# Kernel optimization log

Hardware: AMD Instinct MI355X
Metric: run time of the kernel (lower is better)

The kernel has to match this reference:

```python
import jax, jax.numpy as jnp
import numpy as np

EMB_DIM = 512
QKV_DIM = 512
NUM_HEADS = 8
HEAD_DIM = QKV_DIM // NUM_HEADS
NUM_LANDMARKS = 64
N_ITER = 6


def setup_inputs() -> dict:
    key = jax.random.key(0)
    ks = jax.random.split(key, 9)
    s = 1.0 / np.sqrt(EMB_DIM)
    return {
        "x": jax.random.normal(ks[0], (4, 8192, EMB_DIM), dtype=jnp.float32),
        "Wq": jax.random.normal(ks[1], (EMB_DIM, QKV_DIM), dtype=jnp.float32) * s,
        "bq": jnp.zeros((QKV_DIM,), dtype=jnp.float32),
        "Wk": jax.random.normal(ks[2], (EMB_DIM, QKV_DIM), dtype=jnp.float32) * s,
        "bk": jnp.zeros((QKV_DIM,), dtype=jnp.float32),
        "Wv": jax.random.normal(ks[3], (EMB_DIM, QKV_DIM), dtype=jnp.float32) * s,
        "bv": jnp.zeros((QKV_DIM,), dtype=jnp.float32),
        "Wo": jax.random.normal(ks[4], (QKV_DIM, EMB_DIM), dtype=jnp.float32) * s,
        "bo": jnp.zeros((EMB_DIM,), dtype=jnp.float32),
    }


def _split_heads(x):
    bs, sl, _ = x.shape
    return x.reshape(bs, sl, NUM_HEADS, HEAD_DIM).transpose(0, 2, 1, 3)


def _iterative_inv(K):
    # K: [bs, h, L, L]; Newton-Schulz pseudo-inverse, 'original' init
    L = K.shape[-1]
    I = jnp.eye(L, dtype=K.dtype)
    V = K.swapaxes(-1, -2) / jnp.max(jnp.sum(K, axis=-2))
    for _ in range(N_ITER):
        KV = jnp.matmul(K, V)
        V = jnp.matmul(0.25 * V, 13.0 * I - jnp.matmul(KV, 15.0 * I - jnp.matmul(KV, 7.0 * I - KV)))
    return V


def reference(x, Wq, bq, Wk, bk, Wv, bv, Wo, bo):
    bs, seqlen, _ = x.shape
    # seqlen chosen divisible by NUM_LANDMARKS, so no padding branch
    full_len = seqlen
    q = _split_heads(x @ Wq + bq)
    k = _split_heads(x @ Wk + bk)
    v = _split_heads(x @ Wv + bv)
    scale = 1.0 / np.sqrt(np.sqrt(HEAD_DIM))
    q = q * scale
    k = k * scale

    seg = full_len // NUM_LANDMARKS
    q_land = q.reshape(bs, NUM_HEADS, NUM_LANDMARKS, seg, HEAD_DIM).mean(axis=-2)
    k_land = k.reshape(bs, NUM_HEADS, NUM_LANDMARKS, seg, HEAD_DIM).mean(axis=-2)

    kernel_1 = jax.nn.softmax(jnp.einsum('bhsd,bhld->bhsl', q, k_land), axis=-1)  # [bs,h,S,L]
    kernel_2 = jax.nn.softmax(jnp.einsum('bhld,bhmd->bhlm', q_land, k_land), axis=-1)  # [bs,h,L,L]
    kernel_3 = jax.nn.softmax(jnp.einsum('bhld,bhsd->bhls', q_land, k), axis=-1)  # [bs,h,L,S]

    out = jnp.matmul(jnp.matmul(kernel_1, _iterative_inv(kernel_2)), jnp.matmul(kernel_3, v))  # [bs,h,S,d]
    out = out.transpose(0, 2, 1, 3).reshape(bs, seqlen, QKV_DIM)
    return out @ Wo + bo
```

## Files before the change

kernel.cpp:

```cpp
#include <hip/hip_runtime.h>

#define BS 4
#define SEQL 8192
#define EMB 512
#define NH 8
#define HD 64
#define LM 64
#define SEG 128
#define BH (BS*NH)
#define NCH 16
#define CHS (SEQL/NCH)
#define QSCALE 0.35355339059327373f

typedef unsigned short u16;
typedef __bf16 bf16_t;
typedef __attribute__((ext_vector_type(8))) __bf16 bf16x8;
typedef __attribute__((ext_vector_type(4))) float f32x4;

#define MFMA16(a, b, c) __builtin_amdgcn_mfma_f32_16x16x32_bf16((a), (b), (c), 0, 0, 0)

__device__ __forceinline__ float bf2f(u16 u) {
  return __uint_as_float(((unsigned int)u) << 16);
}
__device__ __forceinline__ u16 f2bf(float f) {
  unsigned int u = __float_as_uint(f);
  u += 0x7fffu + ((u >> 16) & 1u);
  return (u16)(u >> 16);
}
__device__ __forceinline__ float load1_any(const void* p, size_t idx, int isf32) {
  return isf32 ? ((const float*)p)[idx] : bf2f(((const u16*)p)[idx]);
}
__device__ __forceinline__ void load4_any(const void* p, size_t idx, int isf32, float* dst) {
  if (isf32) {
    float4 v = *reinterpret_cast<const float4*>((const float*)p + idx);
    dst[0] = v.x; dst[1] = v.y; dst[2] = v.z; dst[3] = v.w;
  } else {
    ushort4 v = *reinterpret_cast<const ushort4*>((const u16*)p + idx);
    dst[0] = bf2f(v.x); dst[1] = bf2f(v.y); dst[2] = bf2f(v.z); dst[3] = bf2f(v.w);
  }
}
__device__ __forceinline__ void ld8_bf(const void* p, size_t idx, int isf32, u16* o) {
  if (isf32) {
    const float* f = (const float*)p + idx;
    float4 a = *reinterpret_cast<const float4*>(f);
    float4 b = *reinterpret_cast<const float4*>(f + 4);
    o[0] = f2bf(a.x); o[1] = f2bf(a.y); o[2] = f2bf(a.z); o[3] = f2bf(a.w);
    o[4] = f2bf(b.x); o[5] = f2bf(b.y); o[6] = f2bf(b.z); o[7] = f2bf(b.w);
  } else {
    *reinterpret_cast<int4*>(o) = *reinterpret_cast<const int4*>((const u16*)p + idx);
  }
}

__device__ __forceinline__ void async16(const void* g, void* l) {
  __builtin_amdgcn_global_load_lds(
      (const __attribute__((address_space(1))) void*)g,
      (__attribute__((address_space(3))) void*)l, 16, 0, 0);
}

__global__ __launch_bounds__(256) void probe_kernel(const void* x, int* flag) {
  __shared__ int cnt;
  if (threadIdx.x == 0) cnt = 0;
  __syncthreads();
  const u16* p = (const u16*)x;
  int c = 0;
  for (int j = 0; j < 16; j++) {
    u16 u = p[(size_t)(threadIdx.x * 16 + j) * 2];
    int e = (u >> 7) & 0xFF;
    if (e >= 134) c++;
  }
  atomicAdd(&cnt, c);
  __syncthreads();
  if (threadIdx.x == 0) flag[0] = (cnt > 256) ? 1 : 0;
}

__global__ __launch_bounds__(256) void prep_wt_kernel(
    const void* Wq, const void* Wk, const void* Wv, const void* Wo, const int* flag,
    u16* __restrict__ WqT, u16* __restrict__ WkT, u16* __restrict__ WvT, u16* __restrict__ WoT)
{
  __shared__ u16 Ws[64 * 72];
  const int id = blockIdx.x;
  const int z = id >> 6, tile = id & 63;
  const int k0 = (tile >> 3) * 64, n0 = (tile & 7) * 64;
  const void* W = (z == 0) ? Wq : (z == 1) ? Wk : (z == 2) ? Wv : Wo;
  u16* WT = (z == 0) ? WqT : (z == 1) ? WkT : (z == 2) ? WvT : WoT;
  const int isf32 = flag[0];
  const int t = threadIdx.x;
  const int r = t >> 2, cq = (t & 3) * 16;
  u16 tmp[8];
  #pragma unroll
  for (int u = 0; u < 2; u++) {
    ld8_bf(W, (size_t)(k0 + r) * EMB + n0 + cq + 8 * u, isf32, tmp);
    *reinterpret_cast<int4*>(&Ws[r * 72 + cq + 8 * u]) = *reinterpret_cast<int4*>(tmp);
  }
  __syncthreads();
  const int nn = t >> 2, kq = (t & 3) * 16;
  #pragma unroll
  for (int u = 0; u < 2; u++) {
    u16 o[8];
    #pragma unroll
    for (int j = 0; j < 8; j++) o[j] = Ws[(kq + 8 * u + j) * 72 + nn];
    *reinterpret_cast<int4*>(&WT[(size_t)(n0 + nn) * EMB + k0 + kq + 8 * u]) =
        *reinterpret_cast<int4*>(o);
  }
}

__global__ __launch_bounds__(256) void xpart_kernel(const void* x, const int* flag,
                                                    float* __restrict__ xpart,
                                                    u16* __restrict__ xb16) {
  __shared__ float red[512];
  const int blk = blockIdx.x;
  const int bl = blk >> 3, ch = blk & 7;
  const int t = threadIdx.x;
  const int isf32 = flag[0];
  const int rg = t >> 7;
  const int c4 = (t & 127) * 4;
  const size_t base = ((size_t)bl * SEG + ch * 16) * EMB;
  float s0 = 0.f, s1 = 0.f, s2 = 0.f, s3 = 0.f;
  for (int r = rg; r < 16; r += 2) {
    size_t idx = base + (size_t)r * EMB + c4;
    if (isf32) {
      float4 v = *reinterpret_cast<const float4*>((const float*)x + idx);
      ushort4 ob;
      ob.x = f2bf(v.x); ob.y = f2bf(v.y); ob.z = f2bf(v.z); ob.w = f2bf(v.w);
      *reinterpret_cast<ushort4*>(&xb16[idx]) = ob;
      s0 += v.x; s1 += v.y; s2 += v.z; s3 += v.w;
    } else {
      ushort4 v = *reinterpret_cast<const ushort4*>((const u16*)x + idx);
      s0 += bf2f(v.x); s1 += bf2f(v.y); s2 += bf2f(v.z); s3 += bf2f(v.w);
    }
  }
  if (rg == 0) {
    red[c4] = s0; red[c4 + 1] = s1; red[c4 + 2] = s2; red[c4 + 3] = s3;
  }
  __syncthreads();
  if (rg == 1) {
    red[c4] += s0; red[c4 + 1] += s1; red[c4 + 2] += s2; red[c4 + 3] += s3;
  }
  __syncthreads();
  if (t < 128) {
    float4 o;
    o.x = red[t * 4]; o.y = red[t * 4 + 1]; o.z = red[t * 4 + 2]; o.w = red[t * 4 + 3];
    *reinterpret_cast<float4*>(&xpart[(size_t)blk * 512 + t * 4]) = o;
  }
}

__global__ __launch_bounds__(256) void xmean_reduce_kernel(
    const float* __restrict__ xpart, float* __restrict__ xmean) {
  const int bl = blockIdx.x;
  const int t = threadIdx.x;
  const int c = t * 2;
  float s0 = 0.f, s1 = 0.f;
  #pragma unroll
  for (int ch = 0; ch < 8; ch++) {
    const float* p = &xpart[((size_t)(bl * 8 + ch)) * 512 + c];
    s0 += p[0]; s1 += p[1];
  }
  xmean[(size_t)bl * EMB + c]     = s0 * (1.0f / SEG);
  xmean[(size_t)bl * EMB + c + 1] = s1 * (1.0f / SEG);
}

__global__ __launch_bounds__(256) void lm_proj_kernel(
    const float* __restrict__ xmean,
    const void* Wq, const void* bq, const void* Wk, const void* bk,
    const int* flag, float* __restrict__ qL, float* __restrict__ kL,
    u16* __restrict__ qLb, u16* __restrict__ kLb)
{
  __shared__ float As[64 * 17];
  __shared__ float Bs[16 * 64];
  const int t = threadIdx.x;
  const int m0 = blockIdx.x * 64, n0 = blockIdx.y * 64, z = blockIdx.z;
  const void* W    = z ? Wk : Wq;
  const void* bias = z ? bk : bq;
  float* dst       = z ? kL : qL;
  u16*   dstb      = z ? kLb : qLb;
  const int isf32 = flag[0];
  const int tx = t & 15, ty = t >> 4;
  const int arow = t >> 2, akk = (t & 3) << 2;
  const int brow = t >> 4, bcol = (t & 15) << 2;
  float acc[4][4] = {};
  for (int k0 = 0; k0 < EMB; k0 += 16) {
    float4 av = *reinterpret_cast<const float4*>(xmean + (size_t)(m0 + arow) * EMB + k0 + akk);
    As[arow * 17 + akk + 0] = av.x;
    As[arow * 17 + akk + 1] = av.y;
    As[arow * 17 + akk + 2] = av.z;
    As[arow * 17 + akk + 3] = av.w;
    load4_any(W, (size_t)(k0 + brow) * EMB + n0 + bcol, isf32, &Bs[brow * 64 + bcol]);
    __syncthreads();
    #pragma unroll
    for (int kk = 0; kk < 16; kk++) {
      float a[4], b[4];
      #pragma unroll
      for (int i = 0; i < 4; i++) a[i] = As[(ty * 4 + i) * 17 + kk];
      #pragma unroll
      for (int j = 0; j < 4; j++) b[j] = Bs[kk * 64 + tx * 4 + j];
      #pragma unroll
      for (int i = 0; i < 4; i++)
        #pragma unroll
        for (int j = 0; j < 4; j++)
          acc[i][j] = fmaf(a[i], b[j], acc[i][j]);
    }
    __syncthreads();
  }
  #pragma unroll
  for (int i = 0; i < 4; i++) {
    int m = m0 + ty * 4 + i;
    int b = m >> 6, l = m & 63;
    #pragma unroll
    for (int j = 0; j < 4; j++) {
      int n = n0 + tx * 4 + j;
      int h = n >> 6, d = n & 63;
      float c = (acc[i][j] + load1_any(bias, n, isf32)) * QSCALE;
      size_t idx = (size_t)((b * NH + h) * LM + l) * HD + d;
      dst[idx] = c;
      dstb[idx] = f2bf(c);
    }
  }
}

__global__ __launch_bounds__(256, 2) void proj_qkv_fused_kernel(
    const void* x, const u16* __restrict__ xb16, const u16* __restrict__ WqT,
    const u16* __restrict__ WkT, const u16* __restrict__ WvT,
    const void* bq, const void* bk, const void* bv, const int* flag,
    u16* __restrict__ Qb, u16* __restrict__ Kb, u16* __restrict__ VbT)
{
  __shared__ u16 smem[2 * 128 * 64 + 2 * 3 * 64 * 64];
  u16* As = smem;
  u16* Bs = smem + 2 * 128 * 64;
  const int t = threadIdx.x;
  const int orig = blockIdx.x;
  const int swz  = (orig & 7) * 256 + (orig >> 3);
  const int h    = swz & 7;
  const int m0   = (swz >> 3) * 128;
  const int n0   = h * 64;
  const int isf32 = flag[0];
  const u16* xs = isf32 ? xb16 : (const u16*)x;
  const int w = t >> 6, lane = t & 63, q = lane >> 4, c = lane & 15;
  const int wm = (w >> 1) * 64, wn = (w & 1) * 32;
  const int row8 = lane >> 3;
  const int csw  = ((lane & 7) ^ row8) * 8;

  f32x4 acc[3][4][2];
  f32x4 z4 = {0.f, 0.f, 0.f, 0.f};
  #pragma unroll
  for (int z = 0; z < 3; z++)
    #pragma unroll
    for (int mi = 0; mi < 4; mi++) { acc[z][mi][0] = z4; acc[z][mi][1] = z4; }

  #pragma unroll
  for (int u = 0; u < 4; u++) {
    int ca = u * 4 + w;
    async16(&xs[(size_t)(m0 + ca * 8 + row8) * EMB + 0 + csw], &As[ca * 512]);
  }
  #pragma unroll
  for (int u = 0; u < 6; u++) {
    int cb = u * 4 + w, z = cb >> 3, r8 = cb & 7;
    const u16* Wt = (z == 0) ? WqT : (z == 1) ? WkT : WvT;
    async16(&Wt[(size_t)(n0 + r8 * 8 + row8) * EMB + 0 + csw],
            &Bs[z * 4096 + r8 * 512]);
  }
  __syncthreads();

  for (int tt = 0; tt < 8; tt++) {
    const int cur = tt & 1;
    if (tt < 7) {
      const int k1 = (tt + 1) * 64;
      const int nb = (cur ^ 1);
      #pragma unroll
      for (int u = 0; u < 4; u++) {
        int ca = u * 4 + w;
        async16(&xs[(size_t)(m0 + ca * 8 + row8) * EMB + k1 + csw],
                &As[nb * 8192 + ca * 512]);
      }
      #pragma unroll
      for (int u = 0; u < 6; u++) {
        int cb = u * 4 + w, z = cb >> 3, r8 = cb & 7;
        const u16* Wt = (z == 0) ? WqT : (z == 1) ? WkT : WvT;
        async16(&Wt[(size_t)(n0 + r8 * 8 + row8) * EMB + k1 + csw],
                &Bs[nb * 12288 + z * 4096 + r8 * 512]);
      }
    }
    #pragma unroll
    for (int kk = 0; kk < 64; kk += 32) {
      const int u0 = ((((kk >> 3) + q) ^ (c & 7))) * 8;
      bf16x8 af[4];
      #pragma unroll
      for (int mi = 0; mi < 4; mi++)
        af[mi] = *reinterpret_cast<const bf16x8*>(
            &As[cur * 8192 + (wm + mi * 16 + c) * 64 + u0]);
      #pragma unroll
      for (int z = 0; z < 3; z++) {
        bf16x8 b0v = *reinterpret_cast<const bf16x8*>(
            &Bs[cur * 12288 + z * 4096 + (wn + c) * 64 + u0]);
        bf16x8 b1v = *reinterpret_cast<const bf16x8*>(
            &Bs[cur * 12288 + z * 4096 + (wn + 16 + c) * 64 + u0]);
        #pragma unroll
        for (int mi = 0; mi < 4; mi++) {
          acc[z][mi][0] = MFMA16(af[mi], b0v, acc[z][mi][0]);
          acc[z][mi][1] = MFMA16(af[mi], b1v, acc[z][mi][1]);
        }
      }
    }
    __syncthreads();
  }

  float bb[3][2];
  #pragma unroll
  for (int z = 0; z < 3; z++) {
    const void* bias = (z == 0) ? bq : (z == 1) ? bk : bv;
    bb[z][0] = load1_any(bias, n0 + wn + c, isf32);
    bb[z][1] = load1_any(bias, n0 + wn + 16 + c, isf32);
  }
  const int b = m0 >> 13, s0t = m0 & (SEQL - 1);

  #pragma unroll
  for (int z = 0; z < 2; z++) {
    u16* dst = z ? Kb : Qb;
    #pragma unroll
    for (int mi = 0; mi < 4; mi++)
      #pragma unroll
      for (int i = 0; i < 4; i++) {
        int s = s0t + wm + mi * 16 + q * 4 + i;
        size_t rowb = ((size_t)((b * NH + h) * SEQL + s)) * HD;
        dst[rowb + wn + c]      = f2bf((acc[z][mi][0][i] + bb[z][0]) * QSCALE);
        dst[rowb + wn + 16 + c] = f2bf((acc[z][mi][1][i] + bb[z][1]) * QSCALE);
      }
  }

  __syncthreads();
  #pragma unroll
  for (int mi = 0; mi < 4; mi++)
    #pragma unroll
    for (int i = 0; i < 4; i++) {
      int ml = wm + mi * 16 + q * 4 + i;
      smem[(wn + c) * 136 + ml]      = f2bf(acc[2][mi][0][i] + bb[2][0]);
      smem[(wn + 16 + c) * 136 + ml] = f2bf(acc[2][mi][1][i] + bb[2][1]);
    }
  __syncthreads();
  const int nl = t >> 2, cq2 = (t & 3) * 32;
  #pragma unroll
  for (int u = 0; u < 4; u++)
    *reinterpret_cast<int4*>(&VbT[((size_t)((b * NH + h) * HD + nl)) * SEQL + s0t + cq2 + 8 * u]) =
        *reinterpret_cast<int4*>(&smem[nl * 136 + cq2 + 8 * u]);
}

__global__ __launch_bounds__(256) void k2_softmax_kernel(
    const float* __restrict__ qL, const float* __restrict__ kL,
    float* __restrict__ K2, float* __restrict__ cs)
{
  __shared__ float qs[64 * 65], ks[64 * 65], ps[64 * 65];
  const int t = threadIdx.x, bh = blockIdx.x;
  const int r = t >> 2, cb = (t & 3) << 4;
  #pragma unroll
  for (int i = 0; i < 16; i++) {
    qs[r * 65 + cb + i] = qL[((size_t)bh * LM + r) * HD + cb + i];
    ks[r * 65 + cb + i] = kL[((size_t)bh * LM + r) * HD + cb + i];
  }
  __syncthreads();
  float lg[16] = {};
  for (int d = 0; d < HD; d++) {
    float a = qs[r * 65 + d];
    #pragma unroll
    for (int i = 0; i < 16; i++) lg[i] = fmaf(a, ks[(cb + i) * 65 + d], lg[i]);
  }
  float m = lg[0];
  #pragma unroll
  for (int i = 1; i < 16; i++) m = fmaxf(m, lg[i]);
  m = fmaxf(m, __shfl_xor(m, 1));
  m = fmaxf(m, __shfl_xor(m, 2));
  float s = 0.f;
  #pragma unroll
  for (int i = 0; i < 16; i++) { lg[i] = __expf(lg[i] - m); s += lg[i]; }
  s += __shfl_xor(s, 1);
  s += __shfl_xor(s, 2);
  const float inv = 1.0f / s;
  #pragma unroll
  for (int i = 0; i < 16; i++) {
    float p = lg[i] * inv;
    ps[r * 65 + cb + i] = p;
    K2[((size_t)bh * LM + r) * LM + cb + i] = p;
  }
  __syncthreads();
  if (t < 64) {
    float c = 0.f;
    for (int rr = 0; rr < 64; rr++) c += ps[rr * 65 + t];
    cs[bh * LM + t] = c;
  }
}

__device__ __forceinline__ void mm_split(const u16* Ah, const u16* Al,
                                         const u16* Bh, const u16* Bl,
                                         int w, int lane, f32x4* out)
{
  const int q = lane >> 4, c = lane & 15;
  bf16x8 ah[2], al[2];
  #pragma unroll
  for (int k2 = 0; k2 < 2; k2++) {
    ah[k2] = *reinterpret_cast<const bf16x8*>(&Ah[(w * 16 + c) * 72 + k2 * 32 + q * 8]);
    al[k2] = *reinterpret_cast<const bf16x8*>(&Al[(w * 16 + c) * 72 + k2 * 32 + q * 8]);
  }
  #pragma unroll
  for (int nb = 0; nb < 4; nb++) {
    f32x4 acc = {0.f, 0.f, 0.f, 0.f};
    #pragma unroll
    for (int k2 = 0; k2 < 2; k2++) {
      bf16x8 bh_ = *reinterpret_cast<const bf16x8*>(&Bh[(nb * 16 + c) * 72 + k2 * 32 + q * 8]);
      bf16x8 bl_ = *reinterpret_cast<const bf16x8*>(&Bl[(nb * 16 + c) * 72 + k2 * 32 + q * 8]);
      acc = MFMA16(ah[k2], bh_, acc);
      acc = MFMA16(ah[k2], bl_, acc);
      acc = MFMA16(al[k2], bh_, acc);
    }
    out[nb] = acc;
  }
}

__global__ __launch_bounds__(256) void ns_inverse_kernel(
    const float* __restrict__ K2, const float* __restrict__ cs,
    float* __restrict__ Vi)
{
  __shared__ u16 K2h[64 * 72], K2l[64 * 72];
  __shared__ u16 VAh[64 * 72], VAl[64 * 72];
  __shared__ u16 VTh[64 * 72], VTl[64 * 72];
  __shared__ u16 KVh[64 * 72], KVl[64 * 72];
  __shared__ u16 Th [64 * 72], Tl [64 * 72];
  __shared__ float red[256];
  const int t = threadIdx.x, bh = blockIdx.x;
  const int w = t >> 6, lane = t & 63, q = lane >> 4, c = lane & 15;

  float m = -1e30f;
  for (int i = t; i < BH * LM; i += 256) m = fmaxf(m, cs[i]);
  red[t] = m;
  __syncthreads();
  for (int off = 128; off; off >>= 1) {
    if (t < off) red[t] = fmaxf(red[t], red[t + off]);
    __syncthreads();
  }
  const float ginv = 1.0f / red[0];
  __syncthreads();

  {
    const int r = t >> 2, cb = (t & 3) << 4;
    #pragma unroll
    for (int i = 0; i < 16; i++) {
      float v = K2[((size_t)bh * LM + r) * LM + cb + i];
      u16 h1 = f2bf(v);
      K2h[r * 72 + cb + i] = h1;
      K2l[r * 72 + cb + i] = f2bf(v - bf2f(h1));
      float sv = v * ginv;
      u16 h2 = f2bf(sv);
      u16 l2 = f2bf(sv - bf2f(h2));
      VTh[r * 72 + cb + i] = h2;
      VTl[r * 72 + cb + i] = l2;
      VAh[(cb + i) * 72 + r] = h2;
      VAl[(cb + i) * 72 + r] = l2;
    }
  }
  __syncthreads();

  f32x4 o[4];
  for (int it = 0; it < 6; it++) {
    mm_split(K2h, K2l, VTh, VTl, w, lane, o);
    __syncthreads();
    #pragma unroll
    for (int nb = 0; nb < 4; nb++)
      #pragma unroll
      for (int i = 0; i < 4; i++) {
        const int row = w * 16 + q * 4 + i, col = nb * 16 + c;
        const float v = o[nb][i];
        const u16 h1 = f2bf(v);
        KVh[row * 72 + col] = h1;
        KVl[row * 72 + col] = f2bf(v - bf2f(h1));
        const float tv = (row == col ? 7.0f : 0.0f) - v;
        const u16 h2 = f2bf(tv);
        Th[col * 72 + row] = h2;
        Tl[col * 72 + row] = f2bf(tv - bf2f(h2));
      }
    __syncthreads();
    mm_split(KVh, KVl, Th, Tl, w, lane, o);
    __syncthreads();
    #pragma unroll
    for (int nb = 0; nb < 4; nb++)
      #pragma unroll
      for (int i = 0; i < 4; i++) {
        const int row = w * 16 + q * 4 + i, col = nb * 16 + c;
        const float tv = (row == col ? 15.0f : 0.0f) - o[nb][i];
        const u16 h2 = f2bf(tv);
        Th[col * 72 + row] = h2;
        Tl[col * 72 + row] = f2bf(tv - bf2f(h2));
      }
    __syncthreads();
    mm_split(KVh, KVl, Th, Tl, w, lane, o);
    __syncthreads();
    #pragma unroll
    for (int nb = 0; nb < 4; nb++)
      #pragma unroll
      for (int i = 0; i < 4; i++) {
        const int row = w * 16 + q * 4 + i, col = nb * 16 + c;
        const float tv = (row == col ? 13.0f : 0.0f) - o[nb][i];
        const u16 h2 = f2bf(tv);
        Th[col * 72 + row] = h2;
        Tl[col * 72 + row] = f2bf(tv - bf2f(h2));
      }
    __syncthreads();
    mm_split(VAh, VAl, Th, Tl, w, lane, o);
    __syncthreads();
    #pragma unroll
    for (int nb = 0; nb < 4; nb++)
      #pragma unroll
      for (int i = 0; i < 4; i++) {
        const int row = w * 16 + q * 4 + i, col = nb * 16 + c;
        const float v = 0.25f * o[nb][i];
        const u16 h1 = f2bf(v);
        const u16 l1 = f2bf(v - bf2f(h1));
        VAh[row * 72 + col] = h1;
        VAl[row * 72 + col] = l1;
        VTh[col * 72 + row] = h1;
        VTl[col * 72 + row] = l1;
        if (it == 5) Vi[((size_t)bh * LM + row) * LM + col] = v;
      }
    __syncthreads();
  }
}

__global__ __launch_bounds__(256) void k3v_kernel(
    const u16* __restrict__ qLb, const u16* __restrict__ Kb, const u16* __restrict__ VbT,
    float* __restrict__ pnum, float* __restrict__ pden)
{
  __shared__ u16 Ks[64 * 72], Vs[2][64 * 72], Ps[64 * 72];
  __shared__ float denL[256];
  const int t = threadIdx.x, ch = blockIdx.x, bh = blockIdx.y;
  const int w = t >> 6, lane = t & 63, q = lane >> 4, c = lane & 15;
  const int sr = t >> 2, sp = (t & 3) * 16;

  bf16x8 aq[4][2];
  #pragma unroll
  for (int mi = 0; mi < 4; mi++)
    #pragma unroll
    for (int k2 = 0; k2 < 2; k2++)
      aq[mi][k2] = *reinterpret_cast<const bf16x8*>(
          &qLb[((size_t)bh * LM + mi * 16 + c) * HD + k2 * 32 + q * 8]);

  f32x4 z4 = {0.f, 0.f, 0.f, 0.f};
  f32x4 nacc[4];
  #pragma unroll
  for (int mi = 0; mi < 4; mi++) nacc[mi] = z4;
  float denr[16] = {};

  int4 kr0, kr1, vr0, vr1;
  {
    const int s0 = ch * CHS;
    const u16* kp = &Kb[((size_t)bh * SEQL + s0 + sr) * HD + sp];
    const u16* vp = &VbT[((size_t)(bh * HD + sr)) * SEQL + s0 + sp];
    kr0 = *reinterpret_cast<const int4*>(kp);
    kr1 = *reinterpret_cast<const int4*>(kp + 8);
    vr0 = *reinterpret_cast<const int4*>(vp);
    vr1 = *reinterpret_cast<const int4*>(vp + 8);
  }

  for (int sub = 0; sub < 8; sub++) {
    const int cur = sub & 1;
    *reinterpret_cast<int4*>(&Ks[sr * 72 + sp])     = kr0;
    *reinterpret_cast<int4*>(&Ks[sr * 72 + sp + 8]) = kr1;
    *reinterpret_cast<int4*>(&Vs[cur][sr * 72 + sp])     = vr0;
    *reinterpret_cast<int4*>(&Vs[cur][sr * 72 + sp + 8]) = vr1;
    __syncthreads();
    f32x4 sacc[4];
    #pragma unroll
    for (int mi = 0; mi < 4; mi++) sacc[mi] = z4;
    bf16x8 bk0 = *reinterpret_cast<const bf16x8*>(&Ks[(w * 16 + c) * 72 + q * 8]);
    bf16x8 bk1 = *reinterpret_cast<const bf16x8*>(&Ks[(w * 16 + c) * 72 + 32 + q * 8]);
    #pragma unroll
    for (int mi = 0; mi < 4; mi++) {
      sacc[mi] = MFMA16(aq[mi][0], bk0, sacc[mi]);
      sacc[mi] = MFMA16(aq[mi][1], bk1, sacc[mi]);
    }
    #pragma unroll
    for (int mi = 0; mi < 4; mi++)
      #pragma unroll
      for (int i = 0; i < 4; i++) {
        float p = __expf(sacc[mi][i]);
        denr[mi * 4 + i] += p;
        Ps[(mi * 16 + q * 4 + i) * 72 + w * 16 + c] = f2bf(p);
      }
    __syncthreads();
    if (sub < 7) {
      const int s1 = ch * CHS + (sub + 1) * 64;
      const u16* kp = &Kb[((size_t)bh * SEQL + s1 + sr) * HD + sp];
      const u16* vp = &VbT[((size_t)(bh * HD + sr)) * SEQL + s1 + sp];
      kr0 = *reinterpret_cast<const int4*>(kp);
      kr1 = *reinterpret_cast<const int4*>(kp + 8);
      vr0 = *reinterpret_cast<const int4*>(vp);
      vr1 = *reinterpret_cast<const int4*>(vp + 8);
    }
    #pragma unroll
    for (int k2 = 0; k2 < 2; k2++) {
      bf16x8 bv_ = *reinterpret_cast<const bf16x8*>(&Vs[cur][(w * 16 + c) * 72 + k2 * 32 + q * 8]);
      #pragma unroll
      for (int mi = 0; mi < 4; mi++) {
        bf16x8 ap = *reinterpret_cast<const bf16x8*>(&Ps[(mi * 16 + c) * 72 + k2 * 32 + q * 8]);
        nacc[mi] = MFMA16(ap, bv_, nacc[mi]);
      }
    }
  }
  #pragma unroll
  for (int mi = 0; mi < 4; mi++)
    #pragma unroll
    for (int i = 0; i < 4; i++)
      pnum[(((size_t)bh * NCH + ch) * LM + mi * 16 + q * 4 + i) * HD + w * 16 + c] = nacc[mi][i];
  #pragma unroll
  for (int v = 0; v < 16; v++) {
    denr[v] += __shfl_xor(denr[v], 1);
    denr[v] += __shfl_xor(denr[v], 2);
    denr[v] += __shfl_xor(denr[v], 4);
    denr[v] += __shfl_xor(denr[v], 8);
  }
  if (c == 0) {
    #pragma unroll
    for (int mi = 0; mi < 4; mi++)
      #pragma unroll
      for (int i = 0; i < 4; i++)
        denL[w * 64 + mi * 16 + q * 4 + i] = denr[mi * 4 + i];
  }
  __syncthreads();
  if (t < 64)
    pden[((size_t)bh * NCH + ch) * LM + t] = denL[t] + denL[64 + t] + denL[128 + t] + denL[192 + t];
}

__global__ __launch_bounds__(256) void k3v_w2_kernel(
    const float* __restrict__ pnum, const float* __restrict__ pden,
    const float* __restrict__ Vi, u16* __restrict__ W2T)
{
  __shared__ float Vs[64 * 65], Ms[64 * 65], den[64];
  const int t = threadIdx.x, bh = blockIdx.x;
  const int r = t >> 2, cb = (t & 3) << 4;
  #pragma unroll
  for (int i = 0; i < 16; i++) Vs[r * 65 + cb + i] = Vi[((size_t)bh * LM + r) * LM + cb + i];
  float acc[16] = {};
  for (int ch = 0; ch < NCH; ch++) {
    const float* p = pnum + (((size_t)bh * NCH + ch) * LM + r) * HD + cb;
    #pragma unroll
    for (int i = 0; i < 16; i++) acc[i] += p[i];
  }
  if ((t & 3) == 0) {
    float d = 0.f;
    for (int ch = 0; ch < NCH; ch++) d += pden[((size_t)bh * NCH + ch) * LM + r];
    den[r] = d;
  }
  __syncthreads();
  const float dinv = 1.0f / den[r];
  #pragma unroll
  for (int i = 0; i < 16; i++) Ms[r * 65 + cb + i] = acc[i] * dinv;
  __syncthreads();
  float o[16] = {};
  for (int k = 0; k < 64; k++) {
    float a = Vs[r * 65 + k];
    #pragma unroll
    for (int i = 0; i < 16; i++) o[i] = fmaf(a, Ms[k * 65 + cb + i], o[i]);
  }
  #pragma unroll
  for (int i = 0; i < 16; i++)
    W2T[((size_t)bh * HD + cb + i) * LM + r] = f2bf(o[i]);
}

__global__ __launch_bounds__(256) void final_kernel(
    const u16* __restrict__ Qb, const u16* __restrict__ kLb, const u16* __restrict__ W2T,
    u16* __restrict__ pre)
{
  __shared__ u16 Ps[64 * 72];
  __shared__ float smL[256];
  const int t = threadIdx.x, st = blockIdx.x, bh = blockIdx.y;
  const int w = t >> 6, lane = t & 63, q = lane >> 4, c = lane & 15;
  const int sb = st * 64;

  bf16x8 aq[4][2], bkL[2], bw2[2];
  #pragma unroll
  for (int mi = 0; mi < 4; mi++)
    #pragma unroll
    for (int k2 = 0; k2 < 2; k2++)
      aq[mi][k2] = *reinterpret_cast<const bf16x8*>(
          &Qb[((size_t)bh * SEQL + sb + mi * 16 + c) * HD + k2 * 32 + q * 8]);
  #pragma unroll
  for (int k2 = 0; k2 < 2; k2++) {
    bkL[k2] = *reinterpret_cast<const bf16x8*>(
        &kLb[((size_t)bh * LM + w * 16 + c) * HD + k2 * 32 + q * 8]);
    bw2[k2] = *reinterpret_cast<const bf16x8*>(
        &W2T[((size_t)bh * HD + w * 16 + c) * LM + k2 * 32 + q * 8]);
  }

  f32x4 z4 = {0.f, 0.f, 0.f, 0.f};
  f32x4 sacc[4];
  #pragma unroll
  for (int mi = 0; mi < 4; mi++) sacc[mi] = z4;
  #pragma unroll
  for (int k2 = 0; k2 < 2; k2++)
    #pragma unroll
    for (int mi = 0; mi < 4; mi++)
      sacc[mi] = MFMA16(aq[mi][k2], bkL[k2], sacc[mi]);

  float p[16], dn[16];
  #pragma unroll
  for (int v = 0; v < 16; v++) {
    p[v] = __expf(sacc[v >> 2][v & 3]);
    dn[v] = p[v];
  }
  #pragma unroll
  for (int v = 0; v < 16; v++) {
    dn[v] += __shfl_xor(dn[v], 1);
    dn[v] += __shfl_xor(dn[v], 2);
    dn[v] += __shfl_xor(dn[v], 4);
    dn[v] += __shfl_xor(dn[v], 8);
  }
  if (c == 0) {
    #pragma unroll
    for (int mi = 0; mi < 4; mi++)
      #pragma unroll
      for (int i = 0; i < 4; i++)
        smL[w * 64 + mi * 16 + q * 4 + i] = dn[mi * 4 + i];
  }
  #pragma unroll
  for (int mi = 0; mi < 4; mi++)
    #pragma unroll
    for (int i = 0; i < 4; i++)
      Ps[(mi * 16 + q * 4 + i) * 72 + w * 16 + c] = f2bf(p[mi * 4 + i]);
  __syncthreads();

  f32x4 oacc[4];
  #pragma unroll
  for (int mi = 0; mi < 4; mi++) oacc[mi] = z4;
  #pragma unroll
  for (int k2 = 0; k2 < 2; k2++)
    #pragma unroll
    for (int mi = 0; mi < 4; mi++) {
      bf16x8 ap = *reinterpret_cast<const bf16x8*>(&Ps[(mi * 16 + c) * 72 + k2 * 32 + q * 8]);
      oacc[mi] = MFMA16(ap, bw2[k2], oacc[mi]);
    }
  #pragma unroll
  for (int mi = 0; mi < 4; mi++)
    #pragma unroll
    for (int i = 0; i < 4; i++) {
      int row = mi * 16 + q * 4 + i;
      float den = smL[row] + smL[64 + row] + smL[128 + row] + smL[192 + row];
      float v = oacc[mi][i] / den;
      pre[((size_t)((bh >> 3) * SEQL + sb + row)) * EMB + (bh & 7) * HD + w * 16 + c] = f2bf(v);
    }
}

__global__ __launch_bounds__(256, 2) void out_proj_kernel(
    const u16* __restrict__ pre, const u16* __restrict__ WoT, const void* bo,
    const int* flag, void* out)
{
  __shared__ u16 As[2 * 128 * 64];
  __shared__ u16 Bs[2 * 128 * 64];
  const int t = threadIdx.x;
  const int orig = blockIdx.x;
  const int swz  = (orig & 7) * 128 + (orig >> 3);
  const int m0 = (swz >> 2) * 128, n0 = (swz & 3) * 128;
  const int isf32 = flag[0];
  const int w = t >> 6, lane = t & 63, q = lane >> 4, c = lane & 15;
  const int wm = (w >> 1) * 64, wn = (w & 1) * 64;
  const int row8 = lane >> 3;
  const int colsw = ((lane & 7) ^ row8) * 8;

  f32x4 acc[4][4];
  f32x4 z4 = {0.f, 0.f, 0.f, 0.f};
  #pragma unroll
  for (int mi = 0; mi < 4; mi++)
    #pragma unroll
    for (int ni = 0; ni < 4; ni++) acc[mi][ni] = z4;

  #pragma unroll
  for (int u = 0; u < 4; u++) {
    int chA = u * 4 + w;
    async16(&pre[(size_t)(m0 + chA * 8 + row8) * EMB + 0 + colsw], &As[chA * 512]);
    async16(&WoT[(size_t)(n0 + chA * 8 + row8) * EMB + 0 + colsw], &Bs[chA * 512]);
  }
  __syncthreads();

  for (int tt = 0; tt < 8; tt++) {
    const int cur = tt & 1;
    if (tt < 7) {
      const int k1 = (tt + 1) * 64;
      #pragma unroll
      for (int u = 0; u < 4; u++) {
        int chA = u * 4 + w;
        async16(&pre[(size_t)(m0 + chA * 8 + row8) * EMB + k1 + colsw],
                &As[(cur ^ 1) * 8192 + chA * 512]);
        async16(&WoT[(size_t)(n0 + chA * 8 + row8) * EMB + k1 + colsw],
                &Bs[(cur ^ 1) * 8192 + chA * 512]);
      }
    }
    #pragma unroll
    for (int kk = 0; kk < 64; kk += 32) {
      const int u0 = ((((kk >> 3) + q) ^ (c & 7))) * 8;
      bf16x8 af[4], bfv[4];
      #pragma unroll
      for (int mi = 0; mi < 4; mi++)
        af[mi] = *reinterpret_cast<const bf16x8*>(&As[cur * 8192 + (wm + mi * 16 + c) * 64 + u0]);
      #pragma unroll
      for (int ni = 0; ni < 4; ni++)
        bfv[ni] = *reinterpret_cast<const bf16x8*>(&Bs[cur * 8192 + (wn + ni * 16 + c) * 64 + u0]);
      #pragma unroll
      for (int mi = 0; mi < 4; mi++)
        #pragma unroll
        for (int ni = 0; ni < 4; ni++)
          acc[mi][ni] = MFMA16(af[mi], bfv[ni], acc[mi][ni]);
    }
    __syncthreads();
  }
  float bb[4];
  #pragma unroll
  for (int ni = 0; ni < 4; ni++) bb[ni] = load1_any(bo, n0 + wn + ni * 16 + c, isf32);
  #pragma unroll
  for (int mi = 0; mi < 4; mi++)
    #pragma unroll
    for (int i = 0; i < 4; i++) {
      int m = m0 + wm + mi * 16 + q * 4 + i;
      #pragma unroll
      for (int ni = 0; ni < 4; ni++) {
        int n = n0 + wn + ni * 16 + c;
        float v = acc[mi][ni][i] + bb[ni];
        if (isf32) ((float*)out)[(size_t)m * EMB + n] = v;
        else       ((u16*)out)[(size_t)m * EMB + n] = f2bf(v);
      }
    }
}

extern "C" void kernel_launch(void* const* d_in, const int* in_sizes, int n_in,
                              void* d_out, int out_size, void* d_ws, size_t ws_size,
                              hipStream_t stream)
{
  (void)in_sizes; (void)n_in; (void)out_size; (void)ws_size;
  const void* x  = d_in[0];
  const void* Wq = d_in[1];
  const void* bq = d_in[2];
  const void* Wk = d_in[3];
  const void* bk = d_in[4];
  const void* Wv = d_in[5];
  const void* bv = d_in[6];
  const void* Wo = d_in[7];
  const void* bo = d_in[8];

  float* ws = (float*)d_ws;
  int*   flag  = (int*)ws;
  float* xmean = ws + 64;
  float* qL    = xmean + 131072;
  float* kL    = qL + 131072;
  float* K2    = kL + 131072;
  float* cs    = K2 + 131072;
  float* Vi    = cs + 2048;
  float* pnum  = Vi + 131072;
  float* pden  = pnum + 2097152;
  u16* WqT = (u16*)(pden + 32768);
  u16* WkT = WqT + 262144;
  u16* WvT = WkT + 262144;
  u16* WoT = WvT + 262144;
  u16* qLb = WoT + 262144;
  u16* kLb = qLb + 131072;
  u16* W2T = kLb + 131072;
  u16* Qb  = W2T + 131072;
  u16* Kb  = Qb + 16777216;
  u16* VbT = Kb + 16777216;
  u16* xb16 = VbT + 16777216;
  u16* pre = Kb;
  float* xpart = pnum;

  probe_kernel<<<1, 256, 0, stream>>>(x, flag);
  prep_wt_kernel<<<256, 256, 0, stream>>>(Wq, Wk, Wv, Wo, flag, WqT, WkT, WvT, WoT);
  xpart_kernel<<<2048, 256, 0, stream>>>(x, flag, xpart, xb16);
  xmean_reduce_kernel<<<256, 256, 0, stream>>>(xpart, xmean);
  lm_proj_kernel<<<dim3(4, 8, 2), 256, 0, stream>>>(xmean, Wq, bq, Wk, bk, flag, qL, kL, qLb, kLb);
  proj_qkv_fused_kernel<<<dim3(2048), 256, 0, stream>>>(
      x, xb16, WqT, WkT, WvT, bq, bk, bv, flag, Qb, Kb, VbT);
  k2_softmax_kernel<<<BH, 256, 0, stream>>>(qL, kL, K2, cs);
  ns_inverse_kernel<<<BH, 256, 0, stream>>>(K2, cs, Vi);
  k3v_kernel<<<dim3(NCH, BH), 256, 0, stream>>>(qLb, Kb, VbT, pnum, pden);
  k3v_w2_kernel<<<BH, 256, 0, stream>>>(pnum, pden, Vi, W2T);
  final_kernel<<<dim3(SEQL / 64, BH), 256, 0, stream>>>(Qb, kLb, W2T, pre);
  out_proj_kernel<<<dim3(1024), 256, 0, stream>>>(pre, WoT, bo, flag, d_out);
}
```

Before: 383.7 us.

## Stage epilogue stores through LDS for coalesced writes and double-buffer K in k3v

The k3v kernel gets a second K shared-memory buffer and two register prefetch sets, so loads for tile sub+2 are issued two tiles ahead. The final and out_proj kernels now write their results to padded shared memory first and then copy them to global memory with 16-byte vector stores, replacing scattered 2- or 4-byte per-lane writes. This is meant to cut write traffic inefficiency and hide global load latency, at the cost of more LDS, extra barriers and more registers, which could lower occupancy.

```diff
diff --git a/kernel.cpp b/kernel.cpp
--- a/kernel.cpp
+++ b/kernel.cpp
@@ -521,11 +521,22 @@
   }
 }
 
+struct KV2 { int4 k0, k1, v0, v1; };
+__device__ __forceinline__ void k3v_load(const u16* Kb, const u16* VbT, int bh,
+                                         int s0, int sr, int sp, KV2& r) {
+  const u16* kp = &Kb[((size_t)bh * SEQL + s0 + sr) * HD + sp];
+  const u16* vp = &VbT[((size_t)(bh * HD + sr)) * SEQL + s0 + sp];
+  r.k0 = *reinterpret_cast<const int4*>(kp);
+  r.k1 = *reinterpret_cast<const int4*>(kp + 8);
+  r.v0 = *reinterpret_cast<const int4*>(vp);
+  r.v1 = *reinterpret_cast<const int4*>(vp + 8);
+}
+
 __global__ __launch_bounds__(256) void k3v_kernel(
     const u16* __restrict__ qLb, const u16* __restrict__ Kb, const u16* __restrict__ VbT,
     float* __restrict__ pnum, float* __restrict__ pden)
 {
-  __shared__ u16 Ks[64 * 72], Vs[2][64 * 72], Ps[64 * 72];
+  __shared__ u16 Ks[2][64 * 72], Vs[2][64 * 72], Ps[64 * 72];
   __shared__ float denL[256];
   const int t = threadIdx.x, ch = blockIdx.x, bh = blockIdx.y;
   const int w = t >> 6, lane = t & 63, q = lane >> 4, c = lane & 15;
@@ -545,62 +556,55 @@
   for (int mi = 0; mi < 4; mi++) nacc[mi] = z4;
   float denr[16] = {};
 
-  int4 kr0, kr1, vr0, vr1;
-  {
-    const int s0 = ch * CHS;
-    const u16* kp = &Kb[((size_t)bh * SEQL + s0 + sr) * HD + sp];
-    const u16* vp = &VbT[((size_t)(bh * HD + sr)) * SEQL + s0 + sp];
-    kr0 = *reinterpret_cast<const int4*>(kp);
-    kr1 = *reinterpret_cast<const int4*>(kp + 8);
-    vr0 = *reinterpret_cast<const int4*>(vp);
-    vr1 = *reinterpret_cast<const int4*>(vp + 8);
-  }
-
-  for (int sub = 0; sub < 8; sub++) {
-    const int cur = sub & 1;
-    *reinterpret_cast<int4*>(&Ks[sr * 72 + sp])     = kr0;
-    *reinterpret_cast<int4*>(&Ks[sr * 72 + sp + 8]) = kr1;
-    *reinterpret_cast<int4*>(&Vs[cur][sr * 72 + sp])     = vr0;
-    *reinterpret_cast<int4*>(&Vs[cur][sr * 72 + sp + 8]) = vr1;
-    __syncthreads();
-    f32x4 sacc[4];
-    #pragma unroll
-    for (int mi = 0; mi < 4; mi++) sacc[mi] = z4;
-    bf16x8 bk0 = *reinterpret_cast<const bf16x8*>(&Ks[(w * 16 + c) * 72 + q * 8]);
-    bf16x8 bk1 = *reinterpret_cast<const bf16x8*>(&Ks[(w * 16 + c) * 72 + 32 + q * 8]);
-    #pragma unroll
-    for (int mi = 0; mi < 4; mi++) {
-      sacc[mi] = MFMA16(aq[mi][0], bk0, sacc[mi]);
-      sacc[mi] = MFMA16(aq[mi][1], bk1, sacc[mi]);
-    }
-    #pragma unroll
-    for (int mi = 0; mi < 4; mi++)
-      #pragma unroll
-      for (int i = 0; i < 4; i++) {
-        float p = __expf(sacc[mi][i]);
-        denr[mi * 4 + i] += p;
-        Ps[(mi * 16 + q * 4 + i) * 72 + w * 16 + c] = f2bf(p);
-      }
-    __syncthreads();
-    if (sub < 7) {
-      const int s1 = ch * CHS + (sub + 1) * 64;
-      const u16* kp = &Kb[((size_t)bh * SEQL + s1 + sr) * HD + sp];
-      const u16* vp = &VbT[((size_t)(bh * HD + sr)) * SEQL + s1 + sp];
-      kr0 = *reinterpret_cast<const int4*>(kp);
-      kr1 = *reinterpret_cast<const int4*>(kp + 8);
-      vr0 = *reinterpret_cast<const int4*>(vp);
-      vr1 = *reinterpret_cast<const int4*>(vp + 8);
-    }
-    #pragma unroll
-    for (int k2 = 0; k2 < 2; k2++) {
-      bf16x8 bv_ = *reinterpret_cast<const bf16x8*>(&Vs[cur][(w * 16 + c) * 72 + k2 * 32 + q * 8]);
-      #pragma unroll
-      for (int mi = 0; mi < 4; mi++) {
-        bf16x8 ap = *reinterpret_cast<const bf16x8*>(&Ps[(mi * 16 + c) * 72 + k2 * 32 + q * 8]);
-        nacc[mi] = MFMA16(ap, bv_, nacc[mi]);
-      }
-    }
-  }
+  KV2 rA, rB;
+  k3v_load(Kb, VbT, bh, ch * CHS + 0 * 64, sr, sp, rA);
+  k3v_load(Kb, VbT, bh, ch * CHS + 1 * 64, sr, sp, rB);
+
+#define K3V_SUB(SLOT, REGS, NEXTSUB)                                              \
+  {                                                                               \
+    *reinterpret_cast<int4*>(&Ks[SLOT][sr * 72 + sp])     = REGS.k0;              \
+    *reinterpret_cast<int4*>(&Ks[SLOT][sr * 72 + sp + 8]) = REGS.k1;              \
+    *reinterpret_cast<int4*>(&Vs[SLOT][sr * 72 + sp])     = REGS.v0;              \
+    *reinterpret_cast<int4*>(&Vs[SLOT][sr * 72 + sp + 8]) = REGS.v1;              \
+    __syncthreads();                                                              \
+    f32x4 sacc[4];                                                                \
+    _Pragma("unroll")                                                             \
+    for (int mi = 0; mi < 4; mi++) sacc[mi] = z4;                                 \
+    bf16x8 bk0 = *reinterpret_cast<const bf16x8*>(&Ks[SLOT][(w * 16 + c) * 72 + q * 8]);      \
+    bf16x8 bk1 = *reinterpret_cast<const bf16x8*>(&Ks[SLOT][(w * 16 + c) * 72 + 32 + q * 8]); \
+    _Pragma("unroll")                                                             \
+    for (int mi = 0; mi < 4; mi++) {                                              \
+      sacc[mi] = MFMA16(aq[mi][0], bk0, sacc[mi]);                                \
+      sacc[mi] = MFMA16(aq[mi][1], bk1, sacc[mi]);                                \
+    }                                                                             \
+    _Pragma("unroll")                                                             \
+    for (int mi = 0; mi < 4; mi++)                                                \
+      _Pragma("unroll")                                                           \
+      for (int i = 0; i < 4; i++) {                                               \
+        float p = __expf(sacc[mi][i]);                                            \
+        denr[mi * 4 + i] += p;                                                    \
+        Ps[(mi * 16 + q * 4 + i) * 72 + w * 16 + c] = f2bf(p);                    \
+      }                                                                           \
+    __syncthreads();                                                              \
+    if ((NEXTSUB) < 8)                                                            \
+      k3v_load(Kb, VbT, bh, ch * CHS + (NEXTSUB) * 64, sr, sp, REGS);             \
+    _Pragma("unroll")                                                             \
+    for (int k2 = 0; k2 < 2; k2++) {                                              \
+      bf16x8 bv_ = *reinterpret_cast<const bf16x8*>(&Vs[SLOT][(w * 16 + c) * 72 + k2 * 32 + q * 8]); \
+      _Pragma("unroll")                                                           \
+      for (int mi = 0; mi < 4; mi++) {                                            \
+        bf16x8 ap = *reinterpret_cast<const bf16x8*>(&Ps[(mi * 16 + c) * 72 + k2 * 32 + q * 8]);     \
+        nacc[mi] = MFMA16(ap, bv_, nacc[mi]);                                     \
+      }                                                                           \
+    }                                                                             \
+  }
+
+  for (int s2 = 0; s2 < 8; s2 += 2) {
+    K3V_SUB(0, rA, s2 + 2);
+    K3V_SUB(1, rB, s2 + 3);
+  }
+#undef K3V_SUB
+
   #pragma unroll
   for (int mi = 0; mi < 4; mi++)
     #pragma unroll
@@ -666,6 +670,7 @@
     u16* __restrict__ pre)
 {
   __shared__ u16 Ps[64 * 72];
+  __shared__ u16 Co[64 * 72];
   __shared__ float smL[256];
   const int t = threadIdx.x, st = blockIdx.x, bh = blockIdx.y;
   const int w = t >> 6, lane = t & 63, q = lane >> 4, c = lane & 15;
@@ -739,17 +744,26 @@
     for (int i = 0; i < 4; i++) {
       int row = mi * 16 + q * 4 + i;
       float den = smL[row] + smL[64 + row] + smL[128 + row] + smL[192 + row];
-      float v = oacc[mi][i] / den;
-      pre[((size_t)((bh >> 3) * SEQL + sb + row)) * EMB + (bh & 7) * HD + w * 16 + c] = f2bf(v);
-    }
+      Co[row * 72 + w * 16 + c] = f2bf(oacc[mi][i] / den);
+    }
+  __syncthreads();
+  const int rr = t >> 3, l8 = t & 7;
+  #pragma unroll
+  for (int ph = 0; ph < 2; ph++) {
+    int row = ph * 32 + rr;
+    *reinterpret_cast<int4*>(
+        &pre[((size_t)((bh >> 3) * SEQL + sb + row)) * EMB + (bh & 7) * HD + l8 * 8]) =
+        *reinterpret_cast<int4*>(&Co[row * 72 + l8 * 8]);
+  }
 }
 
 __global__ __launch_bounds__(256, 2) void out_proj_kernel(
     const u16* __restrict__ pre, const u16* __restrict__ WoT, const void* bo,
     const int* flag, void* out)
 {
-  __shared__ u16 As[2 * 128 * 64];
-  __shared__ u16 Bs[2 * 128 * 64];
+  __shared__ u16 smem[33792];
+  u16* As = smem;
+  u16* Bs = smem + 16384;
   const int t = threadIdx.x;
   const int orig = blockIdx.x;
   const int swz  = (orig & 7) * 128 + (orig >> 3);
@@ -809,19 +823,54 @@
   float bb[4];
   #pragma unroll
   for (int ni = 0; ni < 4; ni++) bb[ni] = load1_any(bo, n0 + wn + ni * 16 + c, isf32);
-  #pragma unroll
-  for (int mi = 0; mi < 4; mi++)
-    #pragma unroll
-    for (int i = 0; i < 4; i++) {
-      int m = m0 + wm + mi * 16 + q * 4 + i;
-      #pragma unroll
-      for (int ni = 0; ni < 4; ni++) {
-        int n = n0 + wn + ni * 16 + c;
-        float v = acc[mi][ni][i] + bb[ni];
-        if (isf32) ((float*)out)[(size_t)m * EMB + n] = v;
-        else       ((u16*)out)[(size_t)m * EMB + n] = f2bf(v);
-      }
-    }
+
+  if (isf32) {
+    float* Cf = (float*)smem;
+    #pragma unroll
+    for (int mi = 0; mi < 4; mi++)
+      #pragma unroll
+      for (int i = 0; i < 4; i++) {
+        int row = wm + mi * 16 + q * 4 + i;
+        #pragma unroll
+        for (int ni = 0; ni < 4; ni++)
+          Cf[row * 132 + wn + ni * 16 + c] = acc[mi][ni][i] + bb[ni];
+      }
+    __syncthreads();
+    const int rr = t >> 3, l8 = t & 7;
+    #pragma unroll
+    for (int ph = 0; ph < 4; ph++) {
+      int row = ph * 32 + rr;
+      #pragma unroll
+      for (int u = 0; u < 4; u++) {
+        int col = l8 * 4 + u * 32;
+        *reinterpret_cast<float4*>(&((float*)out)[(size_t)(m0 + row) * EMB + n0 + col]) =
+            *reinterpret_cast<const float4*>(&Cf[row * 132 + col]);
+      }
+    }
+  } else {
+    u16* Ct = smem;
+    #pragma unroll
+    for (int mi = 0; mi < 4; mi++)
+      #pragma unroll
+      for (int i = 0; i < 4; i++) {
+        int row = wm + mi * 16 + q * 4 + i;
+        #pragma unroll
+        for (int ni = 0; ni < 4; ni++)
+          Ct[row * 136 + wn + ni * 16 + c] = f2bf(acc[mi][ni][i] + bb[ni]);
+      }
+    __syncthreads();
+    const int rr = t >> 3, l8 = t & 7;
+    #pragma unroll
+    for (int ph = 0; ph < 4; ph++) {
+      int row = ph * 32 + rr;
+      #pragma unroll
+      for (int u = 0; u < 2; u++) {
+        int col = l8 * 8 + u * 64;
+        *reinterpret_cast<int4*>(&((u16*)out)[(size_t)(m0 + row) * EMB + n0 + col]) =
+            *reinterpret_cast<const int4*>(&Ct[row * 136 + col]);
+      }
+    }
+  }
 }
 
 extern "C" void kernel_launch(void* const* d_in, const int* in_sizes, int n_in,
```

Measured after the change: 401.0 us. 4.5% more time.
